# Kernel tuning notes

Measured on AMD Instinct MI355X. Metric: run time of the kernel, lower is better.

Reference implementation:

```python
import jax, jax.numpy as jnp
import numpy as np

N_NODES = 100000


def gcn_conv(x, src, dst, W, b, n_nodes):
    """PyG-style GCNConv: linear transform, symmetric-normalized aggregation with self loops."""
    h = x @ W  # (N, out)
    e = src.shape[0]
    # degree including the implicit self loop (edge weights = 1)
    deg = jax.ops.segment_sum(jnp.ones((e,), dtype=h.dtype), dst, num_segments=n_nodes) + 1.0
    dis = jax.lax.rsqrt(deg)  # deg^{-1/2}
    coef = dis[src] * dis[dst]  # (E,)
    msg = h[src] * coef[:, None]  # (E, out) -- gather + scale
    agg = jax.ops.segment_sum(msg, dst, num_segments=n_nodes)  # scatter-add
    agg = agg + h * (dis * dis)[:, None]  # self-loop contribution
    return agg + b


def setup_inputs() -> dict:
    key = jax.random.key(0)
    k = jax.random.split(key, 6)
    in_dim, hid, out = 128, 128, 64
    E = 1600000
    x = jax.random.normal(k[0], (N_NODES, in_dim), dtype=jnp.float32)
    edge_index = jax.random.randint(k[1], (2, E), 0, N_NODES, dtype=jnp.int64)
    W1 = jax.random.normal(k[2], (in_dim, hid), dtype=jnp.float32) * (1.0 / np.sqrt(in_dim))
    b1 = jnp.zeros((hid,), dtype=jnp.float32)
    W2 = jax.random.normal(k[3], (hid, out), dtype=jnp.float32) * (1.0 / np.sqrt(hid))
    b2 = jnp.zeros((out,), dtype=jnp.float32)
    return {"x": x, "edge_index": edge_index, "W1": W1, "b1": b1, "W2": W2, "b2": b2}


def reference(x, edge_index, W1, b1, W2, b2):
    src, dst = edge_index[0], edge_index[1]
    h = gcn_conv(x, src, dst, W1, b1, N_NODES)
    h = jax.nn.relu(h)
    # dropout is identity in eval mode
    h = gcn_conv(h, src, dst, W2, b2, N_NODES)
    # L2 normalize along feature dim (F.normalize, eps=1e-12)
    norm = jnp.maximum(jnp.linalg.norm(h, axis=-1, keepdims=True), 1e-12)
    return h / norm
```

## Files before the change

kernel.cpp:

```cpp
#include <hip/hip_runtime.h>
#include <hip/hip_bf16.h>
#include <math.h>

#define CSHIFT 9
#define TILE   4096
#define PSH    14
#define PREPB  96

using f16x8 = __attribute__((ext_vector_type(8))) _Float16;
using f16x2 = __attribute__((ext_vector_type(2))) _Float16;
using f32x4 = __attribute__((ext_vector_type(4))) float;
using f32x2 = __attribute__((ext_vector_type(2))) float;

__device__ __forceinline__ unsigned pack_f16(float lo, float hi) {
    auto h = __builtin_amdgcn_cvt_pkrtz(lo, hi);
    return *(unsigned*)&h;
}
__device__ __forceinline__ f16x2 h2(unsigned u) { return *(f16x2*)&u; }
__device__ __forceinline__ f16x2 pshfl_xor(f16x2 a, int m) {
    float f = *(float*)&a;
    f = __shfl_xor(f, m, 64);
    return *(f16x2*)&f;
}

__device__ __forceinline__ unsigned pack_fp8x4(float f0, float f1, float f2, float f3) {
    int w = 0;
    w = __builtin_amdgcn_cvt_pk_fp8_f32(f0, f1, w, false);
    w = __builtin_amdgcn_cvt_pk_fp8_f32(f2, f3, w, true);
    return (unsigned)w;
}
__device__ __forceinline__ void fp8x4_acc2(unsigned v, f32x2& a01, f32x2& a23) {
    a01 += __builtin_amdgcn_cvt_pk_f32_fp8((int)v, false);
    a23 += __builtin_amdgcn_cvt_pk_f32_fp8((int)v, true);
}

__global__ void k_init(int* __restrict__ ccursor, int NC) {
    int i = threadIdx.x;
    if (i < NC) ccursor[i] = 0;
}

__global__ __launch_bounds__(256) void k_part(
    const int* __restrict__ src, const int* __restrict__ dst, int E,
    int* __restrict__ ccursor, int* __restrict__ pairs, int NC, int PB,
    const float* __restrict__ W1, const float* __restrict__ W2,
    unsigned short* __restrict__ wp1, unsigned short* __restrict__ wp2,
    unsigned* __restrict__ g1, unsigned* __restrict__ g2, int N)
{
    if ((int)blockIdx.x >= PB) {
        int idx = (blockIdx.x - PB) * 256 + threadIdx.x;
        if (idx < 32) {
            g1[(size_t)N * 32 + idx] = 0u;
            g2[(size_t)N * 32 + idx] = 0u;
        }
        if (idx < 16384) {
            int e = idx & 7, l = (idx >> 3) & 63, f = idx >> 9;
            int nt = f & 7, kt = f >> 3;
            int k = kt * 32 + (l >> 4) * 8 + e, nn = nt * 16 + (l & 15);
            _Float16 hv = (_Float16)W1[k * 128 + nn];
            wp1[idx] = *(unsigned short*)&hv;
        }
        int i2 = idx - 16384;
        if (i2 >= 0 && i2 < 8192) {
            int e = i2 & 7, l = (i2 >> 3) & 63, f = i2 >> 9;
            int nt = f & 3, kt = f >> 2;
            int k = kt * 32 + (l >> 4) * 8 + e, nn = nt * 16 + (l & 15);
            _Float16 hv = (_Float16)W2[k * 64 + nn];
            wp2[i2] = *(unsigned short*)&hv;
        }
        return;
    }
    __shared__ int sdst[TILE];
    __shared__ int stg[TILE];
    __shared__ unsigned char sbk[TILE];
    __shared__ int h[256], delta[256], cur[256];
    __shared__ int sa[256], sb[256];
    int t = threadIdx.x;
    int base = blockIdx.x * TILE;
    int cnt = min(TILE, E - base);

    h[t] = 0; __syncthreads();
    #pragma unroll
    for (int k = 0; k < TILE / 256; ++k) {
        int e = base + k * 256 + t;
        int d = (e < E) ? dst[e] : -1;
        sdst[k * 256 + t] = d;
        if (d >= 0) atomicAdd(&h[d >> CSHIFT], 1);
    }
    __syncthreads();
    int myc = h[t];
    int* c_ = sa; int* n_ = sb;
    c_[t] = myc; __syncthreads();
    for (int o = 1; o < 256; o <<= 1) {
        int val = c_[t] + ((t >= o) ? c_[t - o] : 0);
        n_[t] = val; __syncthreads();
        int* tmp = c_; c_ = n_; n_ = tmp;
    }
    int ex = c_[t] - myc;
    cur[t] = ex;
    int g = 0;
    if (t < NC && myc) g = atomicAdd(&ccursor[t], myc);
    delta[t] = (t << PSH) + g - ex;
    __syncthreads();

    #pragma unroll
    for (int k = 0; k < TILE / 256; ++k) {
        int e = base + k * 256 + t;
        if (e < E) {
            int d = sdst[k * 256 + t];
            int b = d >> CSHIFT;
            int p = atomicAdd(&cur[b], 1);
            stg[p] = src[e] | ((d & 511) << 17);
            sbk[p] = (unsigned char)b;
        }
    }
    __syncthreads();
    for (int i = t; i < cnt; i += 256)
        pairs[delta[sbk[i]] + i] = stg[i];
}

__global__ __launch_bounds__(256) void k_build(const int* __restrict__ ccursor,
                                               const int* __restrict__ pairs,
                                               int2* __restrict__ seg,
                                               float* __restrict__ dis,
                                               int* __restrict__ csr, int N) {
    __shared__ int h[512];
    __shared__ int cur[512];
    __shared__ int sa[256], sb[256];
    int b = blockIdx.x, t = threadIdx.x;
    h[t] = 0; h[t + 256] = 0; __syncthreads();
    int beg = b << PSH, end = beg + ccursor[b];
    for (int i = beg + t; i < end; i += 256) atomicAdd(&h[pairs[i] >> 17], 1);
    __syncthreads();
    int h0 = h[2 * t], h1 = h[2 * t + 1];
    int p0 = (h0 + 15) & ~15;
    int p1 = (h1 + 15) & ~15;
    int s = p0 + p1;
    int* c_ = sa; int* n_ = sb;
    c_[t] = s; __syncthreads();
    for (int o = 1; o < 256; o <<= 1) {
        int val = c_[t] + ((t >= o) ? c_[t - o] : 0);
        n_[t] = val; __syncthreads();
        int* tmp = c_; c_ = n_; n_ = tmp;
    }
    int ex = c_[t] - s;
    int d0 = b << CSHIFT;
    int da = d0 + 2 * t, db = da + 1;
    cur[2 * t] = ex; cur[2 * t + 1] = ex + p0;
    if (da < N) { seg[da] = make_int2(beg + ex, beg + ex + p0);           dis[da] = rsqrtf((float)h0 + 1.0f); }
    if (db < N) { seg[db] = make_int2(beg + ex + p0, beg + ex + p0 + p1); dis[db] = rsqrtf((float)h1 + 1.0f); }
    for (int i = h0; i < p0; ++i) csr[beg + ex + i] = N;
    for (int i = h1; i < p1; ++i) csr[beg + ex + p0 + i] = N;
    __syncthreads();
    for (int i = beg + t; i < end; i += 256) {
        int pk = pairs[i];
        int p = atomicAdd(&cur[pk >> 17], 1);
        csr[beg + p] = pk & 0x1FFFF;
    }
}

__global__ __launch_bounds__(256) void k_gemm1(
    const float* __restrict__ A, const unsigned short* __restrict__ wp,
    const float* __restrict__ dis, unsigned* __restrict__ G, int M)
{
    constexpr int NT = 8;
    constexpr int ND = 32;

    union UW { uint4 q; f16x8 v; };
    union UA { unsigned u[4]; f16x8 v; };

    const int tid  = threadIdx.x;
    const int wv   = tid >> 6;
    const int lane = tid & 63;
    const int lm   = lane & 15;
    const int lk   = lane >> 4;
    const int m    = blockIdx.x * 64 + wv * 16 + lm;
    const int mc   = m < M ? m : (M - 1);

    f16x8 xf[4];
    {
        const float* Ar = A + (size_t)mc * 128;
        #pragma unroll
        for (int kt = 0; kt < 4; ++kt) {
            int cb = kt * 32 + lk * 8;
            float4 p = *(const float4*)(Ar + cb);
            float4 q = *(const float4*)(Ar + cb + 4);
            UA u;
            u.u[0] = pack_f16(p.x, p.y);
            u.u[1] = pack_f16(p.z, p.w);
            u.u[2] = pack_f16(q.x, q.y);
            u.u[3] = pack_f16(q.z, q.w);
            xf[kt] = u.v;
        }
    }

    f32x4 acc[NT];
    #pragma unroll
    for (int nt = 0; nt < NT; ++nt)
        #pragma unroll
        for (int r = 0; r < 4; ++r) acc[nt][r] = 0.f;

    const uint4* wpv = (const uint4*)wp;
    #pragma unroll
    for (int kt = 0; kt < 4; ++kt) {
        #pragma unroll
        for (int nt = 0; nt < NT; ++nt) {
            UW u; u.q = wpv[(kt * NT + nt) * 64 + lane];
            acc[nt] = __builtin_amdgcn_mfma_f32_16x16x32_f16(
                u.v, xf[kt], acc[nt], 0, 0, 0);
        }
    }

    if (m < M) {
        float dd = dis[m];
        unsigned* gr = G + (size_t)m * ND;
        #pragma unroll
        for (int nt = 0; nt < NT; ++nt)
            gr[nt * 4 + lk] = pack_fp8x4(acc[nt][0] * dd, acc[nt][1] * dd,
                                         acc[nt][2] * dd, acc[nt][3] * dd);
    }
}

__global__ __launch_bounds__(256) void k_agg1(
    const unsigned* __restrict__ g1, const int2* __restrict__ seg,
    const int* __restrict__ csr, const float* __restrict__ dis,
    const float* __restrict__ b1, unsigned* __restrict__ y1, int n)
{
    int wid  = (blockIdx.x * 256 + threadIdx.x) >> 6;
    int lane = threadIdx.x & 63;
    if (wid >= n) return;
    int d  = wid;
    int ll = lane & 31;
    int eh = lane >> 5;
    int2 se = seg[d];
    int beg = se.x, pend = se.y;

    f32x2 a01 = {0.f, 0.f}, a23 = {0.f, 0.f};
    if (eh == 0)
        fp8x4_acc2(g1[(size_t)d * 32 + ll], a01, a23);

    int j = beg;
    for (; j + 32 <= pend; j += 32) {
        unsigned v[16];
        #pragma unroll
        for (int k = 0; k < 16; ++k)
            v[k] = g1[(size_t)csr[j + 2 * k + eh] * 32 + ll];
        #pragma unroll
        for (int k = 0; k < 16; ++k)
            fp8x4_acc2(v[k], a01, a23);
    }
    if (j < pend) {
        unsigned v[8];
        #pragma unroll
        for (int k = 0; k < 8; ++k)
            v[k] = g1[(size_t)csr[j + 2 * k + eh] * 32 + ll];
        #pragma unroll
        for (int k = 0; k < 8; ++k)
            fp8x4_acc2(v[k], a01, a23);
    }

    float a0 = a01[0], a1 = a01[1], a2 = a23[0], a3 = a23[1];
    a0 += __shfl_xor(a0, 32, 64);
    a1 += __shfl_xor(a1, 32, 64);
    a2 += __shfl_xor(a2, 32, 64);
    a3 += __shfl_xor(a3, 32, 64);

    float dd = dis[d];
    float4 bb = *(const float4*)(b1 + 4 * ll);
    float o0 = fmaxf(fmaf(dd, a0, bb.x), 0.f);
    float o1 = fmaxf(fmaf(dd, a1, bb.y), 0.f);
    float o2 = fmaxf(fmaf(dd, a2, bb.z), 0.f);
    float o3 = fmaxf(fmaf(dd, a3, bb.w), 0.f);
    if (lane < 32) {
        uint2 w;
        w.x = pack_f16(o0, o1);
        w.y = pack_f16(o2, o3);
        *((uint2*)(y1 + (size_t)d * 64) + ll) = w;
    }
}

__global__ __launch_bounds__(256) void k_gemm2(
    const unsigned short* __restrict__ A, const unsigned short* __restrict__ wp,
    const float* __restrict__ dis, unsigned* __restrict__ G, int M)
{
    constexpr int NT = 4;
    constexpr int ND = 32;
    union UW { uint4 q; f16x8 v; };

    const int tid  = threadIdx.x;
    const int wv   = tid >> 6;
    const int lane = tid & 63;
    const int lm   = lane & 15;
    const int lk   = lane >> 4;
    const int m0   = blockIdx.x * 128 + wv * 32;

    f16x8 xf[2][4];
    int mrow[2];
    #pragma unroll
    for (int mt = 0; mt < 2; ++mt) {
        int m = m0 + mt * 16 + lm;
        mrow[mt] = m;
        int mc = m < M ? m : (M - 1);
        const uint4* Ar = (const uint4*)(A + (size_t)mc * 128);
        #pragma unroll
        for (int kt = 0; kt < 4; ++kt) {
            UW u; u.q = Ar[kt * 4 + lk];
            xf[mt][kt] = u.v;
        }
    }

    f32x4 acc[2][NT];
    #pragma unroll
    for (int mt = 0; mt < 2; ++mt)
        #pragma unroll
        for (int nt = 0; nt < NT; ++nt)
            #pragma unroll
            for (int r = 0; r < 4; ++r) acc[mt][nt][r] = 0.f;

    const uint4* wpv = (const uint4*)wp;
    #pragma unroll
    for (int kt = 0; kt < 4; ++kt) {
        f16x8 wf[NT];
        #pragma unroll
        for (int nt = 0; nt < NT; ++nt) {
            UW u; u.q = wpv[(kt * NT + nt) * 64 + lane];
            wf[nt] = u.v;
        }
        #pragma unroll
        for (int mt = 0; mt < 2; ++mt)
            #pragma unroll
            for (int nt = 0; nt < NT; ++nt)
                acc[mt][nt] = __builtin_amdgcn_mfma_f32_16x16x32_f16(
                    wf[nt], xf[mt][kt], acc[mt][nt], 0, 0, 0);
    }

    #pragma unroll
    for (int mt = 0; mt < 2; ++mt) {
        int m = mrow[mt];
        if (m < M) {
            float dd = dis[m];
            unsigned* gr = G + (size_t)m * ND;
            #pragma unroll
            for (int nt = 0; nt < NT; ++nt) {
                uint2 w;
                w.x = pack_f16(acc[mt][nt][0] * dd, acc[mt][nt][1] * dd);
                w.y = pack_f16(acc[mt][nt][2] * dd, acc[mt][nt][3] * dd);
                *(uint2*)(gr + nt * 8 + lk * 2) = w;
            }
        }
    }
}

__global__ __launch_bounds__(256) void k_agg2(
    const unsigned* __restrict__ g2, const int2* __restrict__ seg,
    const int* __restrict__ csr, const float* __restrict__ dis,
    const float* __restrict__ b2, float* __restrict__ out, int n)
{
    int wid  = (blockIdx.x * 256 + threadIdx.x) >> 6;
    int lane = threadIdx.x & 63;
    if (wid >= n) return;
    int d  = wid;
    int ol = lane & 7;
    int oh = lane >> 3;
    int2 se = seg[d];
    int beg = se.x, pend = se.y;

    f16x2 A0 = {0, 0}, A1 = {0, 0}, A2 = {0, 0}, A3 = {0, 0};

    int j = beg;
    for (; j + 32 <= pend; j += 32) {
        uint4 v[4];
        #pragma unroll
        for (int k = 0; k < 4; ++k) {
            int s = csr[j + 8 * k + oh];
            v[k] = *((const uint4*)(g2 + (size_t)s * 32) + ol);
        }
        f16x2 p0x = h2(v[0].x) + h2(v[1].x), p1x = h2(v[2].x) + h2(v[3].x);
        f16x2 p0y = h2(v[0].y) + h2(v[1].y), p1y = h2(v[2].y) + h2(v[3].y);
        f16x2 p0z = h2(v[0].z) + h2(v[1].z), p1z = h2(v[2].z) + h2(v[3].z);
        f16x2 p0w = h2(v[0].w) + h2(v[1].w), p1w = h2(v[2].w) + h2(v[3].w);
        A0 += p0x + p1x;
        A1 += p0y + p1y;
        A2 += p0z + p1z;
        A3 += p0w + p1w;
    }
    if (j < pend) {
        uint4 v[2];
        #pragma unroll
        for (int k = 0; k < 2; ++k) {
            int s = csr[j + 8 * k + oh];
            v[k] = *((const uint4*)(g2 + (size_t)s * 32) + ol);
        }
        A0 += h2(v[0].x) + h2(v[1].x);
        A1 += h2(v[0].y) + h2(v[1].y);
        A2 += h2(v[0].z) + h2(v[1].z);
        A3 += h2(v[0].w) + h2(v[1].w);
    }

    #pragma unroll
    for (int o = 8; o <= 32; o <<= 1) {
        A0 += pshfl_xor(A0, o);
        A1 += pshfl_xor(A1, o);
        A2 += pshfl_xor(A2, o);
        A3 += pshfl_xor(A3, o);
    }

    uint4 sv = *((const uint4*)(g2 + (size_t)d * 32) + ol);
    f16x2 sx0 = h2(sv.x), sx1 = h2(sv.y), sx2 = h2(sv.z), sx3 = h2(sv.w);
    float a0 = (float)A0[0] + (float)sx0[0];
    float a1 = (float)A0[1] + (float)sx0[1];
    float a2 = (float)A1[0] + (float)sx1[0];
    float a3 = (float)A1[1] + (float)sx1[1];
    float a4 = (float)A2[0] + (float)sx2[0];
    float a5 = (float)A2[1] + (float)sx2[1];
    float a6 = (float)A3[0] + (float)sx3[0];
    float a7 = (float)A3[1] + (float)sx3[1];

    float dd = dis[d];
    float4 bb0 = *(const float4*)(b2 + 8 * ol);
    float4 bb1 = *(const float4*)(b2 + 8 * ol + 4);
    float v0 = fmaf(dd, a0, bb0.x);
    float v1 = fmaf(dd, a1, bb0.y);
    float v2 = fmaf(dd, a2, bb0.z);
    float v3 = fmaf(dd, a3, bb0.w);
    float v4 = fmaf(dd, a4, bb1.x);
    float v5 = fmaf(dd, a5, bb1.y);
    float v6 = fmaf(dd, a6, bb1.z);
    float v7 = fmaf(dd, a7, bb1.w);

    float ss = v0 * v0 + v1 * v1 + v2 * v2 + v3 * v3
             + v4 * v4 + v5 * v5 + v6 * v6 + v7 * v7;
    ss += __shfl_xor(ss, 1, 64);
    ss += __shfl_xor(ss, 2, 64);
    ss += __shfl_xor(ss, 4, 64);
    float inv = 1.0f / fmaxf(sqrtf(ss), 1e-12f);
    if (oh == 0) {
        float4 w0 = make_float4(v0 * inv, v1 * inv, v2 * inv, v3 * inv);
        float4 w1 = make_float4(v4 * inv, v5 * inv, v6 * inv, v7 * inv);
        *((float4*)(out + (size_t)d * 64 + 8 * ol))     = w0;
        *((float4*)(out + (size_t)d * 64 + 8 * ol + 4)) = w1;
    }
}

extern "C" void kernel_launch(void* const* d_in, const int* in_sizes, int n_in,
                              void* d_out, int out_size, void* d_ws, size_t ws_size,
                              hipStream_t stream) {
    const float* x  = (const float*)d_in[0];
    const int*   ei = (const int*)d_in[1];
    const float* W1 = (const float*)d_in[2];
    const float* b1 = (const float*)d_in[3];
    const float* W2 = (const float*)d_in[4];
    const float* b2 = (const float*)d_in[5];

    const int N = in_sizes[0] / 128;
    const int E = in_sizes[1] / 2;
    const int* src = ei;
    const int* dst = ei + E;
    const int NC = (N + 511) >> CSHIFT;
    const int PB = (E + TILE - 1) / TILE;

    char* ws = (char*)d_ws;
    size_t cur = 0;
    auto alloc = [&](size_t bytes) -> void* {
        void* p = ws + cur;
        cur += (bytes + 255) & ~(size_t)255;
        return p;
    };
    int2*           seg     = (int2*)           alloc((size_t)N * 8);
    int*            ccursor = (int*)            alloc((size_t)NC * 4);
    float*          dis     = (float*)          alloc((size_t)N * 4);
    int*            csr     = (int*)            alloc(((size_t)NC << PSH) * 4);
    int*            pairs   = (int*)            alloc(((size_t)NC << PSH) * 4);
    unsigned short* wp1     = (unsigned short*) alloc(16384 * 2);
    unsigned short* wp2     = (unsigned short*) alloc(8192 * 2);
    unsigned*       g1      = (unsigned*)       alloc((size_t)(N + 1) * 32 * 4);
    unsigned*       y1      = (unsigned*)       alloc((size_t)N * 64 * 4);
    unsigned*       g2      = (unsigned*)       alloc((size_t)(N + 1) * 32 * 4);
    float*          out     = (float*)d_out;

    k_init<<<1, 256, 0, stream>>>(ccursor, NC);
    k_part<<<PB + PREPB, 256, 0, stream>>>(src, dst, E, ccursor, pairs, NC, PB,
                                           W1, W2, wp1, wp2, g1, g2, N);
    k_build<<<NC, 256, 0, stream>>>(ccursor, pairs, seg, dis, csr, N);

    k_gemm1<<<(N + 63) / 64, 256, 0, stream>>>(x, wp1, dis, g1, N);
    k_agg1<<<(N * 64 + 255) / 256, 256, 0, stream>>>(g1, seg, csr, dis, b1, y1, N);
    k_gemm2<<<(N + 127) / 128, 256, 0, stream>>>((const unsigned short*)y1, wp2, dis, g2, N);
    k_agg2<<<(N * 64 + 255) / 256, 256, 0, stream>>>(g2, seg, csr, dis, b2, out, N);
}
```

Baseline: 159.1 us.

## Fuse layer-1 aggregation with layer-2 GEMM via LDS and last-wave-done MFMA

```diff
diff --git a/kernel.cpp b/kernel.cpp
--- a/kernel.cpp
+++ b/kernel.cpp
@@ -220,132 +220,114 @@
     }
 }
 
-__global__ __launch_bounds__(256) void k_agg1(
+__global__ __launch_bounds__(1024) void k_agg1g(
     const unsigned* __restrict__ g1, const int2* __restrict__ seg,
     const int* __restrict__ csr, const float* __restrict__ dis,
-    const float* __restrict__ b1, unsigned* __restrict__ y1, int n)
+    const float* __restrict__ b1, const unsigned short* __restrict__ wp2,
+    unsigned* __restrict__ g2, int n)
 {
-    int wid  = (blockIdx.x * 256 + threadIdx.x) >> 6;
-    int lane = threadIdx.x & 63;
-    if (wid >= n) return;
-    int d  = wid;
-    int ll = lane & 31;
-    int eh = lane >> 5;
-    int2 se = seg[d];
-    int beg = se.x, pend = se.y;
-
-    f32x2 a01 = {0.f, 0.f}, a23 = {0.f, 0.f};
-    if (eh == 0)
-        fp8x4_acc2(g1[(size_t)d * 32 + ll], a01, a23);
-
-    int j = beg;
-    for (; j + 32 <= pend; j += 32) {
-        unsigned v[16];
-        #pragma unroll
-        for (int k = 0; k < 16; ++k)
-            v[k] = g1[(size_t)csr[j + 2 * k + eh] * 32 + ll];
-        #pragma unroll
-        for (int k = 0; k < 16; ++k)
-            fp8x4_acc2(v[k], a01, a23);
-    }
-    if (j < pend) {
-        unsigned v[8];
-        #pragma unroll
-        for (int k = 0; k < 8; ++k)
-            v[k] = g1[(size_t)csr[j + 2 * k + eh] * 32 + ll];
-        #pragma unroll
-        for (int k = 0; k < 8; ++k)
-            fp8x4_acc2(v[k], a01, a23);
-    }
-
-    float a0 = a01[0], a1 = a01[1], a2 = a23[0], a3 = a23[1];
-    a0 += __shfl_xor(a0, 32, 64);
-    a1 += __shfl_xor(a1, 32, 64);
-    a2 += __shfl_xor(a2, 32, 64);
-    a3 += __shfl_xor(a3, 32, 64);
-
-    float dd = dis[d];
-    float4 bb = *(const float4*)(b1 + 4 * ll);
-    float o0 = fmaxf(fmaf(dd, a0, bb.x), 0.f);
-    float o1 = fmaxf(fmaf(dd, a1, bb.y), 0.f);
-    float o2 = fmaxf(fmaf(dd, a2, bb.z), 0.f);
-    float o3 = fmaxf(fmaf(dd, a3, bb.w), 0.f);
-    if (lane < 32) {
-        uint2 w;
-        w.x = pack_f16(o0, o1);
-        w.y = pack_f16(o2, o3);
-        *((uint2*)(y1 + (size_t)d * 64) + ll) = w;
-    }
-}
-
-__global__ __launch_bounds__(256) void k_gemm2(
-    const unsigned short* __restrict__ A, const unsigned short* __restrict__ wp,
-    const float* __restrict__ dis, unsigned* __restrict__ G, int M)
-{
-    constexpr int NT = 4;
-    constexpr int ND = 32;
     union UW { uint4 q; f16x8 v; };
-
-    const int tid  = threadIdx.x;
-    const int wv   = tid >> 6;
-    const int lane = tid & 63;
-    const int lm   = lane & 15;
-    const int lk   = lane >> 4;
-    const int m0   = blockIdx.x * 128 + wv * 32;
-
-    f16x8 xf[2][4];
-    int mrow[2];
-    #pragma unroll
-    for (int mt = 0; mt < 2; ++mt) {
-        int m = m0 + mt * 16 + lm;
-        mrow[mt] = m;
-        int mc = m < M ? m : (M - 1);
-        const uint4* Ar = (const uint4*)(A + (size_t)mc * 128);
+    union UB { unsigned u[4]; f16x8 v; };
+    __shared__ unsigned ylds[16][68];
+    __shared__ float sdis[16];
+    __shared__ int scnt;
+
+    const int w    = threadIdx.x >> 6;
+    const int lane = threadIdx.x & 63;
+    const int d0   = blockIdx.x * 16;
+    const int d    = d0 + w;
+
+    if (threadIdx.x == 0) scnt = 0;
+    __syncthreads();
+
+    if (d < n) {
+        int ll = lane & 31;
+        int eh = lane >> 5;
+        int2 se = seg[d];
+        int beg = se.x, pend = se.y;
+
+        f32x2 a01 = {0.f, 0.f}, a23 = {0.f, 0.f};
+        if (eh == 0)
+            fp8x4_acc2(g1[(size_t)d * 32 + ll], a01, a23);
+
+        int j = beg;
+        for (; j + 32 <= pend; j += 32) {
+            unsigned v[16];
+            #pragma unroll
+            for (int k = 0; k < 16; ++k)
+                v[k] = g1[(size_t)csr[j + 2 * k + eh] * 32 + ll];
+            #pragma unroll
+            for (int k = 0; k < 16; ++k)
+                fp8x4_acc2(v[k], a01, a23);
+        }
+        if (j < pend) {
+            unsigned v[8];
+            #pragma unroll
+            for (int k = 0; k < 8; ++k)
+                v[k] = g1[(size_t)csr[j + 2 * k + eh] * 32 + ll];
+            #pragma unroll
+            for (int k = 0; k < 8; ++k)
+                fp8x4_acc2(v[k], a01, a23);
+        }
+
+        float a0 = a01[0], a1 = a01[1], a2 = a23[0], a3 = a23[1];
+        a0 += __shfl_xor(a0, 32, 64);
+        a1 += __shfl_xor(a1, 32, 64);
+        a2 += __shfl_xor(a2, 32, 64);
+        a3 += __shfl_xor(a3, 32, 64);
+
+        float dd = dis[d];
+        float4 bb = *(const float4*)(b1 + 4 * ll);
+        float o0 = fmaxf(fmaf(dd, a0, bb.x), 0.f);
+        float o1 = fmaxf(fmaf(dd, a1, bb.y), 0.f);
+        float o2 = fmaxf(fmaf(dd, a2, bb.z), 0.f);
+        float o3 = fmaxf(fmaf(dd, a3, bb.w), 0.f);
+        if (lane < 32) {
+            ylds[w][2 * ll]     = pack_f16(o0, o1);
+            ylds[w][2 * ll + 1] = pack_f16(o2, o3);
+        }
+        if (lane == 0) sdis[w] = dd;
+    } else {
+        if (lane < 32) { ylds[w][2 * lane] = 0u; ylds[w][2 * lane + 1] = 0u; }
+        if (lane == 0) sdis[w] = 0.f;
+    }
+
+    __threadfence_block();
+    int old = 0;
+    if (lane == 0) old = atomicAdd(&scnt, 1);
+    old = __shfl(old, 0, 64);
+    if (old != 15) return;
+
+    __threadfence_block();
+    const int lm = lane & 15;
+    const int lk = lane >> 4;
+    const uint4* wpv = (const uint4*)wp2;
+
+    f16x8 yf[4];
+    #pragma unroll
+    for (int kt = 0; kt < 4; ++kt) {
+        UB ub;
+        #pragma unroll
+        for (int i = 0; i < 4; ++i)
+            ub.u[i] = ylds[lm][kt * 16 + lk * 4 + i];
+        yf[kt] = ub.v;
+    }
+
+    float dd = sdis[lm];
+    #pragma unroll
+    for (int nt = 0; nt < 4; ++nt) {
+        f32x4 acc = {0.f, 0.f, 0.f, 0.f};
         #pragma unroll
         for (int kt = 0; kt < 4; ++kt) {
-            UW u; u.q = Ar[kt * 4 + lk];
-            xf[mt][kt] = u.v;
-        }
-    }
-
-    f32x4 acc[2][NT];
-    #pragma unroll
-    for (int mt = 0; mt < 2; ++mt)
-        #pragma unroll
-        for (int nt = 0; nt < NT; ++nt)
-            #pragma unroll
-            for (int r = 0; r < 4; ++r) acc[mt][nt][r] = 0.f;
-
-    const uint4* wpv = (const uint4*)wp;
-    #pragma unroll
-    for (int kt = 0; kt < 4; ++kt) {
-        f16x8 wf[NT];
-        #pragma unroll
-        for (int nt = 0; nt < NT; ++nt) {
-            UW u; u.q = wpv[(kt * NT + nt) * 64 + lane];
-            wf[nt] = u.v;
-        }
-        #pragma unroll
-        for (int mt = 0; mt < 2; ++mt)
-            #pragma unroll
-            for (int nt = 0; nt < NT; ++nt)
-                acc[mt][nt] = __builtin_amdgcn_mfma_f32_16x16x32_f16(
-                    wf[nt], xf[mt][kt], acc[mt][nt], 0, 0, 0);
-    }
-
-    #pragma unroll
-    for (int mt = 0; mt < 2; ++mt) {
-        int m = mrow[mt];
-        if (m < M) {
-            float dd = dis[m];
-            unsigned* gr = G + (size_t)m * ND;
-            #pragma unroll
-            for (int nt = 0; nt < NT; ++nt) {
-                uint2 w;
-                w.x = pack_f16(acc[mt][nt][0] * dd, acc[mt][nt][1] * dd);
-                w.y = pack_f16(acc[mt][nt][2] * dd, acc[mt][nt][3] * dd);
-                *(uint2*)(gr + nt * 8 + lk * 2) = w;
-            }
+            UW uw; uw.q = wpv[(kt * 4 + nt) * 64 + lane];
+            acc = __builtin_amdgcn_mfma_f32_16x16x32_f16(uw.v, yf[kt], acc, 0, 0, 0);
+        }
+        int row = d0 + lm;
+        if (row < n) {
+            uint2 wv2;
+            wv2.x = pack_f16(acc[0] * dd, acc[1] * dd);
+            wv2.y = pack_f16(acc[2] * dd, acc[3] * dd);
+            *(uint2*)(g2 + (size_t)row * 32 + nt * 8 + lk * 2) = wv2;
         }
     }
 }
@@ -473,7 +455,6 @@
     unsigned short* wp1     = (unsigned short*) alloc(16384 * 2);
     unsigned short* wp2     = (unsigned short*) alloc(8192 * 2);
     unsigned*       g1      = (unsigned*)       alloc((size_t)(N + 1) * 32 * 4);
-    unsigned*       y1      = (unsigned*)       alloc((size_t)N * 64 * 4);
     unsigned*       g2      = (unsigned*)       alloc((size_t)(N + 1) * 32 * 4);
     float*          out     = (float*)d_out;
 
@@ -483,7 +464,6 @@
     k_build<<<NC, 256, 0, stream>>>(ccursor, pairs, seg, dis, csr, N);
 
     k_gemm1<<<(N + 63) / 64, 256, 0, stream>>>(x, wp1, dis, g1, N);
-    k_agg1<<<(N * 64 + 255) / 256, 256, 0, stream>>>(g1, seg, csr, dis, b1, y1, N);
-    k_gemm2<<<(N + 127) / 128, 256, 0, stream>>>((const unsigned short*)y1, wp2, dis, g2, N);
+    k_agg1g<<<(N + 15) / 16, 1024, 0, stream>>>(g1, seg, csr, dis, b1, wp2, g2, N);
     k_agg2<<<(N * 64 + 255) / 256, 256, 0, stream>>>(g2, seg, csr, dis, b2, out, N);
 }
```

Result: slower. 171.2 us (+7.6%).
